# Kernel optimization log

Hardware: AMD Instinct MI355X
Metric: run time of the kernel (lower is better)

## Reference

```python
import jax, jax.numpy as jnp
import numpy as np

B = 131072
IN_DIM = 21   # velocity_dim * (past_frame + 2) = 3 * 7
HID = 512
OUT_DIM = 21  # 7 waypoints * 3 coords
SEG = 0.5     # segment width in in_same_segment
WW = 0.5      # rescale weight for same-segment elements
INVALID = -10000.0
VALID_THRESH = -5000.0


def setup_inputs() -> dict:
    key = jax.random.key(0)
    ks = jax.random.split(key, 9)
    velocities = jax.random.normal(ks[0], (B, IN_DIM), dtype=jnp.float32)
    gt = jax.random.normal(ks[1], (B, 7, 3), dtype=jnp.float32)
    # emulate warp_gt padding: some trailing waypoints are invalid sentinels
    pad_mask = jax.random.bernoulli(ks[2], 0.2, (B, 7, 1))
    gt = jnp.where(pad_mask, jnp.float32(INVALID), gt)
    s1 = 1.0 / np.sqrt(IN_DIM)
    s2 = 1.0 / np.sqrt(HID)
    W1 = jax.random.uniform(ks[3], (HID, IN_DIM), jnp.float32, -s1, s1)
    b1 = jax.random.uniform(ks[4], (HID,), jnp.float32, -s1, s1)
    W2 = jax.random.uniform(ks[5], (HID, HID), jnp.float32, -s2, s2)
    b2 = jax.random.uniform(ks[6], (HID,), jnp.float32, -s2, s2)
    W3 = jax.random.uniform(ks[7], (OUT_DIM, HID), jnp.float32, -s2, s2)
    b3 = jax.random.uniform(ks[8], (OUT_DIM,), jnp.float32, -s2, s2)
    return {"velocities": velocities, "gt": gt,
            "W1": W1, "b1": b1, "W2": W2, "b2": b2, "W3": W3, "b3": b3}


def reference(velocities, gt, W1, b1, W2, b2, W3, b3):
    # plan_head MLP: 21 -> 512 -> 512 -> 21
    h = jax.nn.relu(velocities @ W1.T + b1)
    h = jax.nn.relu(h @ W2.T + b2)
    out = h @ W3.T + b3                      # [B, 21]
    pred = out.reshape(-1, 7, 3)             # waypoints x1..x7, 3 coords each
    # segment-conditional weighted L1 loss (vectorized form of the Python loop)
    valid = gt > VALID_THRESH
    same_seg = jnp.floor(pred / SEG) == jnp.floor(gt / SEG)
    w = jnp.where(valid & same_seg, jnp.float32(WW), jnp.float32(1.0))
    diff = jnp.abs(pred * w - gt * w)
    num = jnp.sum(jnp.where(valid, diff, 0.0))
    den = jnp.sum(valid.astype(jnp.float32))
    return num / den
```

## Files before the change

### kernel.cpp

```cpp
#include <hip/hip_runtime.h>
#include <hip/hip_bf16.h>

typedef __bf16 bf16_t;
typedef __bf16 bf16x8 __attribute__((ext_vector_type(8)));
typedef float f32x4 __attribute__((ext_vector_type(4)));

#define IN_DIM 21
#define HID 512
#define OUT_DIM 21
#define M_TILE 64
#define LSTRIDE 520
#define THREADS 1024

__global__ void prep_kernel(const float* __restrict__ W1, const float* __restrict__ W2,
                            const float* __restrict__ W3,
                            bf16_t* __restrict__ W1f, bf16_t* __restrict__ W2f,
                            bf16_t* __restrict__ W3f) {
    int i = blockIdx.x * blockDim.x + threadIdx.x;
    int stride = gridDim.x * blockDim.x;
    const int NW2 = HID * HID;
    const int NW1 = 32 * 512;
    const int NW3 = 16 * 2 * 512;
    for (; i < NW2 + NW1 + NW3; i += stride) {
        if (i < NW2) {
            int j = i & 7, lane = (i >> 3) & 63, ntile = (i >> 9) & 31, kstep = i >> 14;
            int n = ntile * 16 + (lane & 15);
            int k = kstep * 32 + (lane >> 4) * 8 + j;
            W2f[i] = (bf16_t)W2[n * HID + k];
        } else if (i < NW2 + NW1) {
            int t = i - NW2;
            int j = t & 7, lane = (t >> 3) & 63, ntile = t >> 9;
            int n = ntile * 16 + (lane & 15);
            int k = (lane >> 4) * 8 + j;
            W1f[t] = (k < IN_DIM) ? (bf16_t)W1[n * IN_DIM + k] : (bf16_t)0.0f;
        } else {
            int t = i - NW2 - NW1;
            int j = t & 7, lane = (t >> 3) & 63, ot = (t >> 9) & 1, kstep = t >> 10;
            int o = ot * 16 + (lane & 15);
            int k = kstep * 32 + (lane >> 4) * 8 + j;
            W3f[t] = (o < OUT_DIM) ? (bf16_t)W3[o * HID + k] : (bf16_t)0.0f;
        }
    }
}

__global__ __launch_bounds__(THREADS)
void fused_kernel(const float* __restrict__ V, const float* __restrict__ gt,
                  const float* __restrict__ b1, const float* __restrict__ b2,
                  const float* __restrict__ b3,
                  const bf16_t* __restrict__ W1f, const bf16_t* __restrict__ W2f,
                  const bf16_t* __restrict__ W3f, float* __restrict__ accum) {
    __shared__ __align__(16) bf16_t vlds[M_TILE][32];
    __shared__ __align__(16) bf16_t h1[M_TILE][LSTRIDE];
    __shared__ __align__(16) bf16_t h2[M_TILE][LSTRIDE];
    __shared__ float redbuf[32];

    const int tid  = threadIdx.x;
    const int wave = tid >> 6;
    const int lane = tid & 63;
    const int quad = lane >> 4;
    const int l16  = lane & 15;
    const long row0 = (long)blockIdx.x * M_TILE;

    for (int idx = tid; idx < M_TILE * 32; idx += THREADS) {
        int r = idx >> 5, c = idx & 31;
        float v = (c < IN_DIM) ? V[(row0 + r) * IN_DIM + c] : 0.0f;
        vlds[r][c] = (bf16_t)v;
    }
    __syncthreads();

    {
        bf16x8 a[4];
        #pragma unroll
        for (int mt = 0; mt < 4; ++mt)
            a[mt] = *reinterpret_cast<const bf16x8*>(&vlds[mt * 16 + l16][quad * 8]);
        #pragma unroll
        for (int nt = 0; nt < 2; ++nt) {
            int ntile = wave * 2 + nt;
            int n = ntile * 16 + l16;
            bf16x8 b = *reinterpret_cast<const bf16x8*>(W1f + ntile * 512 + lane * 8);
            float bias = b1[n];
            #pragma unroll
            for (int mt = 0; mt < 4; ++mt) {
                f32x4 c = {0.0f, 0.0f, 0.0f, 0.0f};
                c = __builtin_amdgcn_mfma_f32_16x16x32_bf16(a[mt], b, c, 0, 0, 0);
                #pragma unroll
                for (int r = 0; r < 4; ++r) {
                    float v = c[r] + bias;
                    v = v > 0.0f ? v : 0.0f;
                    h1[mt * 16 + quad * 4 + r][n] = (bf16_t)v;
                }
            }
        }
    }
    __syncthreads();

    {
        f32x4 acc[4][2];
        #pragma unroll
        for (int mt = 0; mt < 4; ++mt)
            #pragma unroll
            for (int nt = 0; nt < 2; ++nt)
                acc[mt][nt] = (f32x4){0.0f, 0.0f, 0.0f, 0.0f};

        const bf16_t* w2p0 = W2f + (wave * 2 + 0) * 512 + lane * 8;
        const bf16_t* w2p1 = W2f + (wave * 2 + 1) * 512 + lane * 8;

        for (int ks = 0; ks < 16; ++ks) {
            bf16x8 b0 = *reinterpret_cast<const bf16x8*>(w2p0 + ks * 32 * 512);
            bf16x8 b1v = *reinterpret_cast<const bf16x8*>(w2p1 + ks * 32 * 512);
            bf16x8 a[4];
            #pragma unroll
            for (int mt = 0; mt < 4; ++mt)
                a[mt] = *reinterpret_cast<const bf16x8*>(&h1[mt * 16 + l16][ks * 32 + quad * 8]);
            #pragma unroll
            for (int mt = 0; mt < 4; ++mt) {
                acc[mt][0] = __builtin_amdgcn_mfma_f32_16x16x32_bf16(a[mt], b0, acc[mt][0], 0, 0, 0);
                acc[mt][1] = __builtin_amdgcn_mfma_f32_16x16x32_bf16(a[mt], b1v, acc[mt][1], 0, 0, 0);
            }
        }

        #pragma unroll
        for (int nt = 0; nt < 2; ++nt) {
            int n = wave * 32 + nt * 16 + l16;
            float bias = b2[n];
            #pragma unroll
            for (int mt = 0; mt < 4; ++mt) {
                #pragma unroll
                for (int r = 0; r < 4; ++r) {
                    float v = acc[mt][nt][r] + bias;
                    v = v > 0.0f ? v : 0.0f;
                    h2[mt * 16 + quad * 4 + r][n] = (bf16_t)v;
                }
            }
        }
    }
    __syncthreads();

    if (wave < 8) {
        const int mt = wave >> 1;
        const int ot = wave & 1;
        f32x4 acc3 = {0.0f, 0.0f, 0.0f, 0.0f};
        for (int ks = 0; ks < 16; ++ks) {
            bf16x8 a = *reinterpret_cast<const bf16x8*>(&h2[mt * 16 + l16][ks * 32 + quad * 8]);
            bf16x8 b = *reinterpret_cast<const bf16x8*>(W3f + (ks * 2 + ot) * 512 + lane * 8);
            acc3 = __builtin_amdgcn_mfma_f32_16x16x32_bf16(a, b, acc3, 0, 0, 0);
        }

        float num = 0.0f, den = 0.0f;
        int col = ot * 16 + l16;
        if (col < OUT_DIM) {
            float bias = b3[col];
            #pragma unroll
            for (int r = 0; r < 4; ++r) {
                long grow = row0 + mt * 16 + quad * 4 + r;
                float pred = acc3[r] + bias;
                float g = gt[grow * OUT_DIM + col];
                if (g > -5000.0f) {
                    float w = (floorf(pred * 2.0f) == floorf(g * 2.0f)) ? 0.5f : 1.0f;
                    num += fabsf(pred * w - g * w);
                    den += 1.0f;
                }
            }
        }
        #pragma unroll
        for (int off = 32; off > 0; off >>= 1) {
            num += __shfl_down(num, off);
            den += __shfl_down(den, off);
        }
        if (lane == 0) { redbuf[wave * 2] = num; redbuf[wave * 2 + 1] = den; }
    }
    __syncthreads();
    if (tid == 0) {
        float n8 = 0.0f, d8 = 0.0f;
        #pragma unroll
        for (int w = 0; w < 8; ++w) { n8 += redbuf[w * 2]; d8 += redbuf[w * 2 + 1]; }
        atomicAdd(accum, n8);
        atomicAdd(accum + 1, d8);
    }
}

__global__ void finalize_kernel(const float* __restrict__ accum, float* __restrict__ out) {
    if (threadIdx.x == 0) out[0] = accum[0] / accum[1];
}

extern "C" void kernel_launch(void* const* d_in, const int* in_sizes, int n_in,
                              void* d_out, int out_size, void* d_ws, size_t ws_size,
                              hipStream_t stream) {
    const float* V  = (const float*)d_in[0];
    const float* gt = (const float*)d_in[1];
    const float* W1 = (const float*)d_in[2];
    const float* b1 = (const float*)d_in[3];
    const float* W2 = (const float*)d_in[4];
    const float* b2 = (const float*)d_in[5];
    const float* W3 = (const float*)d_in[6];
    const float* b3 = (const float*)d_in[7];
    float* out = (float*)d_out;

    char* ws = (char*)d_ws;
    float* accum = (float*)ws;
    bf16_t* W2f = (bf16_t*)(ws + 16);
    bf16_t* W1f = (bf16_t*)(ws + 16 + 512 * 512 * 2);
    bf16_t* W3f = (bf16_t*)(ws + 16 + 512 * 512 * 2 + 32 * 512 * 2);

    int Brows = in_sizes[0] / IN_DIM;
    int grid = Brows / M_TILE;

    hipMemsetAsync(accum, 0, 2 * sizeof(float), stream);
    prep_kernel<<<576, 512, 0, stream>>>(W1, W2, W3, W1f, W2f, W3f);
    fused_kernel<<<grid, THREADS, 0, stream>>>(V, gt, b1, b2, b3, W1f, W2f, W3f, accum);
    finalize_kernel<<<1, 64, 0, stream>>>(accum, out);
}
```

Before: 194.1 us.

## Swizzle LDS activations, software-pipeline W2 loads, and split layer-3 accumulators

Replaces the padded LDS row stride for h1/h2 with an XOR swizzle of column groups by row, which avoids bank conflicts and shrinks shared memory. The layer-2 loop is fully unrolled with a triple-buffered register prefetch of W2 fragments two steps ahead and a double-buffered prefetch of h1 fragments. Layer 3 issues the gt loads before the MFMA loop and uses two independent accumulators to break the MFMA dependency chain. A launch-bounds occupancy hint of 4 is added, which may force register spilling given the extra prefetch buffers.

```diff
diff --git a/kernel.cpp b/kernel.cpp
--- a/kernel.cpp
+++ b/kernel.cpp
@@ -9,8 +9,11 @@
 #define HID 512
 #define OUT_DIM 21
 #define M_TILE 64
-#define LSTRIDE 520
 #define THREADS 1024
+
+__device__ __forceinline__ int swz(int row, int col) {
+    return col ^ ((row & 7) << 3);
+}
 
 __global__ void prep_kernel(const float* __restrict__ W1, const float* __restrict__ W2,
                             const float* __restrict__ W3,
@@ -43,15 +46,15 @@
     }
 }
 
-__global__ __launch_bounds__(THREADS)
+__global__ __launch_bounds__(THREADS, 4)
 void fused_kernel(const float* __restrict__ V, const float* __restrict__ gt,
                   const float* __restrict__ b1, const float* __restrict__ b2,
                   const float* __restrict__ b3,
                   const bf16_t* __restrict__ W1f, const bf16_t* __restrict__ W2f,
                   const bf16_t* __restrict__ W3f, float* __restrict__ accum) {
-    __shared__ __align__(16) bf16_t vlds[M_TILE][32];
-    __shared__ __align__(16) bf16_t h1[M_TILE][LSTRIDE];
-    __shared__ __align__(16) bf16_t h2[M_TILE][LSTRIDE];
+    __shared__ __align__(16) bf16_t vlds[M_TILE][40];
+    __shared__ __align__(16) bf16_t h1[M_TILE][HID];
+    __shared__ __align__(16) bf16_t h2[M_TILE][HID];
     __shared__ float redbuf[32];
 
     const int tid  = threadIdx.x;
@@ -87,7 +90,8 @@
                 for (int r = 0; r < 4; ++r) {
                     float v = c[r] + bias;
                     v = v > 0.0f ? v : 0.0f;
-                    h1[mt * 16 + quad * 4 + r][n] = (bf16_t)v;
+                    int m = mt * 16 + quad * 4 + r;
+                    h1[m][swz(m, n)] = (bf16_t)v;
                 }
             }
         }
@@ -102,21 +106,41 @@
             for (int nt = 0; nt < 2; ++nt)
                 acc[mt][nt] = (f32x4){0.0f, 0.0f, 0.0f, 0.0f};
 
-        const bf16_t* w2p0 = W2f + (wave * 2 + 0) * 512 + lane * 8;
-        const bf16_t* w2p1 = W2f + (wave * 2 + 1) * 512 + lane * 8;
-
+        const bf16_t* w2p = W2f + (wave * 2) * 512 + lane * 8;
+
+        bf16x8 b0buf[3], b1buf[3];
+        bf16x8 ac[4], an[4];
+        #pragma unroll
+        for (int p = 0; p < 2; ++p) {
+            b0buf[p] = *reinterpret_cast<const bf16x8*>(w2p + p * 16384);
+            b1buf[p] = *reinterpret_cast<const bf16x8*>(w2p + p * 16384 + 512);
+        }
+        #pragma unroll
+        for (int mt = 0; mt < 4; ++mt) {
+            int rr = mt * 16 + l16;
+            ac[mt] = *reinterpret_cast<const bf16x8*>(&h1[rr][swz(rr, quad * 8)]);
+        }
+
+        #pragma unroll
         for (int ks = 0; ks < 16; ++ks) {
-            bf16x8 b0 = *reinterpret_cast<const bf16x8*>(w2p0 + ks * 32 * 512);
-            bf16x8 b1v = *reinterpret_cast<const bf16x8*>(w2p1 + ks * 32 * 512);
-            bf16x8 a[4];
-            #pragma unroll
-            for (int mt = 0; mt < 4; ++mt)
-                a[mt] = *reinterpret_cast<const bf16x8*>(&h1[mt * 16 + l16][ks * 32 + quad * 8]);
+            if (ks + 2 < 16) {
+                b0buf[(ks + 2) % 3] = *reinterpret_cast<const bf16x8*>(w2p + (ks + 2) * 16384);
+                b1buf[(ks + 2) % 3] = *reinterpret_cast<const bf16x8*>(w2p + (ks + 2) * 16384 + 512);
+            }
+            if (ks + 1 < 16) {
+                #pragma unroll
+                for (int mt = 0; mt < 4; ++mt) {
+                    int rr = mt * 16 + l16;
+                    an[mt] = *reinterpret_cast<const bf16x8*>(&h1[rr][swz(rr, (ks + 1) * 32 + quad * 8)]);
+                }
+            }
             #pragma unroll
             for (int mt = 0; mt < 4; ++mt) {
-                acc[mt][0] = __builtin_amdgcn_mfma_f32_16x16x32_bf16(a[mt], b0, acc[mt][0], 0, 0, 0);
-                acc[mt][1] = __builtin_amdgcn_mfma_f32_16x16x32_bf16(a[mt], b1v, acc[mt][1], 0, 0, 0);
-            }
+                acc[mt][0] = __builtin_amdgcn_mfma_f32_16x16x32_bf16(ac[mt], b0buf[ks % 3], acc[mt][0], 0, 0, 0);
+                acc[mt][1] = __builtin_amdgcn_mfma_f32_16x16x32_bf16(ac[mt], b1buf[ks % 3], acc[mt][1], 0, 0, 0);
+            }
+            #pragma unroll
+            for (int mt = 0; mt < 4; ++mt) ac[mt] = an[mt];
         }
 
         #pragma unroll
@@ -129,7 +153,8 @@
                 for (int r = 0; r < 4; ++r) {
                     float v = acc[mt][nt][r] + bias;
                     v = v > 0.0f ? v : 0.0f;
-                    h2[mt * 16 + quad * 4 + r][n] = (bf16_t)v;
+                    int m = mt * 16 + quad * 4 + r;
+                    h2[m][swz(m, n)] = (bf16_t)v;
                 }
             }
         }
@@ -139,25 +164,41 @@
     if (wave < 8) {
         const int mt = wave >> 1;
         const int ot = wave & 1;
-        f32x4 acc3 = {0.0f, 0.0f, 0.0f, 0.0f};
-        for (int ks = 0; ks < 16; ++ks) {
-            bf16x8 a = *reinterpret_cast<const bf16x8*>(&h2[mt * 16 + l16][ks * 32 + quad * 8]);
-            bf16x8 b = *reinterpret_cast<const bf16x8*>(W3f + (ks * 2 + ot) * 512 + lane * 8);
-            acc3 = __builtin_amdgcn_mfma_f32_16x16x32_bf16(a, b, acc3, 0, 0, 0);
-        }
-
-        float num = 0.0f, den = 0.0f;
-        int col = ot * 16 + l16;
-        if (col < OUT_DIM) {
-            float bias = b3[col];
+        const int col = ot * 16 + l16;
+        const bool colv = (col < OUT_DIM);
+
+        float g[4];
+        float bias3 = 0.0f;
+        if (colv) {
+            bias3 = b3[col];
             #pragma unroll
             for (int r = 0; r < 4; ++r) {
                 long grow = row0 + mt * 16 + quad * 4 + r;
-                float pred = acc3[r] + bias;
-                float g = gt[grow * OUT_DIM + col];
-                if (g > -5000.0f) {
-                    float w = (floorf(pred * 2.0f) == floorf(g * 2.0f)) ? 0.5f : 1.0f;
-                    num += fabsf(pred * w - g * w);
+                g[r] = gt[grow * OUT_DIM + col];
+            }
+        }
+
+        f32x4 acc3a = {0.0f, 0.0f, 0.0f, 0.0f};
+        f32x4 acc3b = {0.0f, 0.0f, 0.0f, 0.0f};
+        const int rr = mt * 16 + l16;
+        #pragma unroll
+        for (int ks = 0; ks < 16; ks += 2) {
+            bf16x8 a0 = *reinterpret_cast<const bf16x8*>(&h2[rr][swz(rr, ks * 32 + quad * 8)]);
+            bf16x8 a1 = *reinterpret_cast<const bf16x8*>(&h2[rr][swz(rr, (ks + 1) * 32 + quad * 8)]);
+            bf16x8 bb0 = *reinterpret_cast<const bf16x8*>(W3f + (ks * 2 + ot) * 512 + lane * 8);
+            bf16x8 bb1 = *reinterpret_cast<const bf16x8*>(W3f + ((ks + 1) * 2 + ot) * 512 + lane * 8);
+            acc3a = __builtin_amdgcn_mfma_f32_16x16x32_bf16(a0, bb0, acc3a, 0, 0, 0);
+            acc3b = __builtin_amdgcn_mfma_f32_16x16x32_bf16(a1, bb1, acc3b, 0, 0, 0);
+        }
+
+        float num = 0.0f, den = 0.0f;
+        if (colv) {
+            #pragma unroll
+            for (int r = 0; r < 4; ++r) {
+                float pred = acc3a[r] + acc3b[r] + bias3;
+                if (g[r] > -5000.0f) {
+                    float w = (floorf(pred * 2.0f) == floorf(g[r] * 2.0f)) ? 0.5f : 1.0f;
+                    num += fabsf(pred * w - g[r] * w);
                     den += 1.0f;
                 }
             }
```

After: 186.5 us. 3.9% less time.

## Swap MFMA operands, use 512-thread blocks with single swizzled LDS buffer

Applied to the files above, without the earlier changes.

Weights now go in as the MFMA A operand and activations as B, so each lane holds four consecutive output features and can write packed bf16x4 stores into a single XOR-swizzled LDS activation buffer. Using one buffer instead of h1/h2 roughly halves LDS use, and the block shrinks to 512 threads with each wave computing 4x4 tiles, which raises register reuse of the loaded weight fragments. The intent is fewer LDS bank conflicts and store instructions, more resident blocks per CU, and more MFMA work per global weight load. The costs are an extra barrier before h is overwritten, higher register pressure from 16 accumulators, and a fully unrolled K loop.

```diff
diff --git a/kernel.cpp b/kernel.cpp
--- a/kernel.cpp
+++ b/kernel.cpp
@@ -2,6 +2,7 @@
 #include <hip/hip_bf16.h>
 
 typedef __bf16 bf16_t;
+typedef __bf16 bf16x4 __attribute__((ext_vector_type(4)));
 typedef __bf16 bf16x8 __attribute__((ext_vector_type(8)));
 typedef float f32x4 __attribute__((ext_vector_type(4)));
 
@@ -9,8 +10,11 @@
 #define HID 512
 #define OUT_DIM 21
 #define M_TILE 64
-#define LSTRIDE 520
-#define THREADS 1024
+#define THREADS 512
+
+__device__ __forceinline__ int swz(int row, int col) {
+    return col ^ ((row & 7) << 3);
+}
 
 __global__ void prep_kernel(const float* __restrict__ W1, const float* __restrict__ W2,
                             const float* __restrict__ W3,
@@ -43,22 +47,22 @@
     }
 }
 
-__global__ __launch_bounds__(THREADS)
+__global__ __launch_bounds__(THREADS, 4)
 void fused_kernel(const float* __restrict__ V, const float* __restrict__ gt,
                   const float* __restrict__ b1, const float* __restrict__ b2,
                   const float* __restrict__ b3,
                   const bf16_t* __restrict__ W1f, const bf16_t* __restrict__ W2f,
                   const bf16_t* __restrict__ W3f, float* __restrict__ accum) {
-    __shared__ __align__(16) bf16_t vlds[M_TILE][32];
-    __shared__ __align__(16) bf16_t h1[M_TILE][LSTRIDE];
-    __shared__ __align__(16) bf16_t h2[M_TILE][LSTRIDE];
-    __shared__ float redbuf[32];
+    __shared__ __align__(16) bf16_t vlds[M_TILE][40];
+    __shared__ __align__(16) bf16_t h[M_TILE][HID];
+    __shared__ float redbuf[16];
 
     const int tid  = threadIdx.x;
     const int wave = tid >> 6;
     const int lane = tid & 63;
     const int quad = lane >> 4;
     const int l16  = lane & 15;
+    const int sx   = (l16 & 7) << 3;
     const long row0 = (long)blockIdx.x * M_TILE;
 
     for (int idx = tid; idx < M_TILE * 32; idx += THREADS) {
@@ -69,95 +73,117 @@
     __syncthreads();
 
     {
-        bf16x8 a[4];
+        bf16x8 bv[4];
         #pragma unroll
         for (int mt = 0; mt < 4; ++mt)
-            a[mt] = *reinterpret_cast<const bf16x8*>(&vlds[mt * 16 + l16][quad * 8]);
-        #pragma unroll
-        for (int nt = 0; nt < 2; ++nt) {
-            int ntile = wave * 2 + nt;
-            int n = ntile * 16 + l16;
-            bf16x8 b = *reinterpret_cast<const bf16x8*>(W1f + ntile * 512 + lane * 8);
-            float bias = b1[n];
+            bv[mt] = *reinterpret_cast<const bf16x8*>(&vlds[mt * 16 + l16][quad * 8]);
+        #pragma unroll
+        for (int nt = 0; nt < 4; ++nt) {
+            int ntile = wave * 4 + nt;
+            bf16x8 aw = *reinterpret_cast<const bf16x8*>(W1f + ntile * 512 + lane * 8);
+            f32x4 bias = *reinterpret_cast<const f32x4*>(b1 + ntile * 16 + quad * 4);
+            int n0 = ntile * 16 + quad * 4;
             #pragma unroll
             for (int mt = 0; mt < 4; ++mt) {
                 f32x4 c = {0.0f, 0.0f, 0.0f, 0.0f};
-                c = __builtin_amdgcn_mfma_f32_16x16x32_bf16(a[mt], b, c, 0, 0, 0);
+                c = __builtin_amdgcn_mfma_f32_16x16x32_bf16(aw, bv[mt], c, 0, 0, 0);
+                bf16x4 pk;
                 #pragma unroll
                 for (int r = 0; r < 4; ++r) {
-                    float v = c[r] + bias;
-                    v = v > 0.0f ? v : 0.0f;
-                    h1[mt * 16 + quad * 4 + r][n] = (bf16_t)v;
+                    float v = c[r] + bias[r];
+                    pk[r] = (bf16_t)(v > 0.0f ? v : 0.0f);
                 }
+                int m = mt * 16 + l16;
+                *reinterpret_cast<bf16x4*>(&h[m][n0 ^ sx]) = pk;
             }
         }
     }
     __syncthreads();
 
     {
-        f32x4 acc[4][2];
+        f32x4 acc[4][4];
         #pragma unroll
         for (int mt = 0; mt < 4; ++mt)
             #pragma unroll
-            for (int nt = 0; nt < 2; ++nt)
+            for (int nt = 0; nt < 4; ++nt)
                 acc[mt][nt] = (f32x4){0.0f, 0.0f, 0.0f, 0.0f};
 
-        const bf16_t* w2p0 = W2f + (wave * 2 + 0) * 512 + lane * 8;
-        const bf16_t* w2p1 = W2f + (wave * 2 + 1) * 512 + lane * 8;
-
+        const bf16_t* w2p = W2f + (wave * 4) * 512 + lane * 8;
+
+        #pragma unroll
         for (int ks = 0; ks < 16; ++ks) {
-            bf16x8 b0 = *reinterpret_cast<const bf16x8*>(w2p0 + ks * 32 * 512);
-            bf16x8 b1v = *reinterpret_cast<const bf16x8*>(w2p1 + ks * 32 * 512);
-            bf16x8 a[4];
+            bf16x8 bh[4];
             #pragma unroll
             for (int mt = 0; mt < 4; ++mt)
-                a[mt] = *reinterpret_cast<const bf16x8*>(&h1[mt * 16 + l16][ks * 32 + quad * 8]);
+                bh[mt] = *reinterpret_cast<const bf16x8*>(
+                    &h[mt * 16 + l16][(ks * 32 + quad * 8) ^ sx]);
+            bf16x8 aw[4];
+            #pragma unroll
+            for (int nt = 0; nt < 4; ++nt)
+                aw[nt] = *reinterpret_cast<const bf16x8*>(w2p + ks * 16384 + nt * 512);
+            #pragma unroll
+            for (int mt = 0; mt < 4; ++mt)
+                #pragma unroll
+                for (int nt = 0; nt < 4; ++nt)
+                    acc[mt][nt] = __builtin_amdgcn_mfma_f32_16x16x32_bf16(aw[nt], bh[mt], acc[mt][nt], 0, 0, 0);
+        }
+        __syncthreads();
+
+        #pragma unroll
+        for (int nt = 0; nt < 4; ++nt) {
+            int ntile = wave * 4 + nt;
+            f32x4 bias = *reinterpret_cast<const f32x4*>(b2 + ntile * 16 + quad * 4);
+            int n0 = ntile * 16 + quad * 4;
             #pragma unroll
             for (int mt = 0; mt < 4; ++mt) {
-                acc[mt][0] = __builtin_amdgcn_mfma_f32_16x16x32_bf16(a[mt], b0, acc[mt][0], 0, 0, 0);
-                acc[mt][1] = __builtin_amdgcn_mfma_f32_16x16x32_bf16(a[mt], b1v, acc[mt][1], 0, 0, 0);
-            }
-        }
-
-        #pragma unroll
-        for (int nt = 0; nt < 2; ++nt) {
-            int n = wave * 32 + nt * 16 + l16;
-            float bias = b2[n];
-            #pragma unroll
-            for (int mt = 0; mt < 4; ++mt) {
+                bf16x4 pk;
                 #pragma unroll
                 for (int r = 0; r < 4; ++r) {
-                    float v = acc[mt][nt][r] + bias;
-                    v = v > 0.0f ? v : 0.0f;
-                    h2[mt * 16 + quad * 4 + r][n] = (bf16_t)v;
+                    float v = acc[mt][nt][r] + bias[r];
+                    pk[r] = (bf16_t)(v > 0.0f ? v : 0.0f);
                 }
+                int m = mt * 16 + l16;
+                *reinterpret_cast<bf16x4*>(&h[m][n0 ^ sx]) = pk;
             }
         }
     }
     __syncthreads();
 
-    if (wave < 8) {
+    {
         const int mt = wave >> 1;
         const int ot = wave & 1;
-        f32x4 acc3 = {0.0f, 0.0f, 0.0f, 0.0f};
-        for (int ks = 0; ks < 16; ++ks) {
-            bf16x8 a = *reinterpret_cast<const bf16x8*>(&h2[mt * 16 + l16][ks * 32 + quad * 8]);
-            bf16x8 b = *reinterpret_cast<const bf16x8*>(W3f + (ks * 2 + ot) * 512 + lane * 8);
-            acc3 = __builtin_amdgcn_mfma_f32_16x16x32_bf16(a, b, acc3, 0, 0, 0);
+        const int o0 = ot * 16 + quad * 4;
+        const long grow = row0 + mt * 16 + l16;
+
+        float g[4], b3v[4];
+        #pragma unroll
+        for (int r = 0; r < 4; ++r) {
+            bool v = (o0 + r) < OUT_DIM;
+            g[r]   = v ? gt[grow * OUT_DIM + o0 + r] : -10000.0f;
+            b3v[r] = v ? b3[o0 + r] : 0.0f;
+        }
+
+        f32x4 acc3a = {0.0f, 0.0f, 0.0f, 0.0f};
+        f32x4 acc3b = {0.0f, 0.0f, 0.0f, 0.0f};
+        const int rr = mt * 16 + l16;
+        #pragma unroll
+        for (int ks = 0; ks < 16; ks += 2) {
+            bf16x8 bh0 = *reinterpret_cast<const bf16x8*>(&h[rr][(ks * 32 + quad * 8) ^ sx]);
+            bf16x8 bh1 = *reinterpret_cast<const bf16x8*>(&h[rr][((ks + 1) * 32 + quad * 8) ^ sx]);
+            bf16x8 aw0 = *reinterpret_cast<const bf16x8*>(W3f + (ks * 2 + ot) * 512 + lane * 8);
+            bf16x8 aw1 = *reinterpret_cast<const bf16x8*>(W3f + ((ks + 1) * 2 + ot) * 512 + lane * 8);
+            acc3a = __builtin_amdgcn_mfma_f32_16x16x32_bf16(aw0, bh0, acc3a, 0, 0, 0);
+            acc3b = __builtin_amdgcn_mfma_f32_16x16x32_bf16(aw1, bh1, acc3b, 0, 0, 0);
         }
 
         float num = 0.0f, den = 0.0f;
-        int col = ot * 16 + l16;
-        if (col < OUT_DIM) {
-            float bias = b3[col];
-            #pragma unroll
-            for (int r = 0; r < 4; ++r) {
-                long grow = row0 + mt * 16 + quad * 4 + r;
-                float pred = acc3[r] + bias;
-                float g = gt[grow * OUT_DIM + col];
-                if (g > -5000.0f) {
-                    float w = (floorf(pred * 2.0f) == floorf(g * 2.0f)) ? 0.5f : 1.0f;
-                    num += fabsf(pred * w - g * w);
+        #pragma unroll
+        for (int r = 0; r < 4; ++r) {
+            if ((o0 + r) < OUT_DIM) {
+                float pred = acc3a[r] + acc3b[r] + b3v[r];
+                if (g[r] > -5000.0f) {
+                    float w = (floorf(pred * 2.0f) == floorf(g[r] * 2.0f)) ? 0.5f : 1.0f;
+                    num += fabsf(pred * w - g[r] * w);
                     den += 1.0f;
                 }
             }
```

Result: slower. 222.7 us (+14.8%).
